# Performance work log

Measured on AMD Instinct MI355X. Metric: run time of the kernel, lower is better.

Reference implementation:

```python
import jax, jax.numpy as jnp
import numpy as np
import math

# config constants (match init_kwargs)
N_HEAD = 16
KNN_NUM = 4
MEM_FRAC = 4.0
BOOKKEEPING_FRAC = 0.0
RESID_ONLY = False
RESID_FOUND = 0.5   # set_resid_frac(resid_frac): found/current mix
RESID_CURR = 0.5
KNN_INFLUENCE = 1.0
NEG_INF = jnp.finfo(jnp.float32).min


def setup_inputs() -> dict:
    key = jax.random.key(0)
    k1, k2, k3, k4, k5 = jax.random.split(key, 5)
    B, T, C = 1, 2048, 1024
    H, d = N_HEAD, C // N_HEAD
    M = 8192  # per-head memory-store entries
    return {
        "x": jax.random.normal(k1, (B, T, C), jnp.float32),
        "c_attn_w": jax.random.normal(k2, (3 * C, C), jnp.float32) * 0.02,
        "c_proj_w": jax.random.normal(k3, (C, C), jnp.float32) * 0.02,
        "key_store": jax.random.normal(k4, (H, M, d), jnp.float32),
        "value_store": jax.random.normal(k5, (H, M, d), jnp.float32),
    }


def _knn_get(att, k, q, v, key_store, value_store):
    # att: (B,H,T,T), k/q/v: (B,H,T,d), stores: (H,M,d). B must be 1 (original
    # scatter offset i*t is only consistent for b==1).
    B, H, T, d = k.shape
    scale = 1.0 / math.sqrt(d)
    att_last = att[:, :, -1, :]                     # (B,H,T) last-query column
    # bookkeeping_frac == 0.0 -> skipped; mem_frac truthy -> threshold filter
    mask = att_last >= (1.0 / (MEM_FRAC * T))       # nonzero after zeroing

    # per-head flattened token lists, shape (H, N=B*T, d)
    kh = jnp.swapaxes(k, 0, 1).reshape(H, B * T, d)
    qh = jnp.swapaxes(q, 0, 1).reshape(H, B * T, d)
    vh = jnp.swapaxes(v, 0, 1).reshape(H, B * T, d)
    mask_h = jnp.swapaxes(mask, 0, 1).reshape(H, B * T)

    # exact L2 kNN (FAISS IndexFlatL2 equivalent): d2[h,n,m] = ||kh - ks||^2
    d2 = (jnp.sum(kh * kh, -1)[:, :, None]
          - 2.0 * jnp.einsum('hnd,hmd->hnm', kh, key_store)
          + jnp.sum(key_store * key_store, -1)[:, None, :])
    _, idx = jax.lax.top_k(-d2, KNN_NUM)            # (H,N,K) nearest indices

    h_ix = jnp.arange(H)[:, None, None]
    keys_found = key_store[h_ix, idx]               # (H,N,K,d)
    vals_found = value_store[h_ix, idx]
    keys_found = jnp.moveaxis(keys_found, 2, 0)     # (K,H,N,d)
    vals_found = jnp.moveaxis(vals_found, 2, 0)
    if not RESID_ONLY:
        keys_found = jnp.concatenate([kh[None], keys_found], axis=0)  # (K+1,H,N,d)
        vals_found = jnp.concatenate([vh[None], vals_found], axis=0)

    attf = jnp.einsum('khnd,hnd->khn', keys_found, qh) * scale
    attf = jnp.where(jnp.isnan(attf), NEG_INF, attf)
    attf = jax.nn.softmax(attf * KNN_INFLUENCE, axis=0)
    vals_new = jnp.einsum('khn,khnd->hnd', attf, vals_found)
    if RESID_FOUND > 0 or RESID_CURR > 0:
        vals_new = vals_new * RESID_FOUND + vh * RESID_CURR

    v_out = jnp.where(mask_h[..., None], vals_new, vh)   # scatter-equivalent
    return jnp.swapaxes(v_out.reshape(H, B, T, d), 0, 1)  # (B,H,T,d)


def reference(x, c_attn_w, c_proj_w, key_store, value_store):
    B, T, C = x.shape
    H, d = N_HEAD, C // N_HEAD
    qkv = x @ c_attn_w.T                             # (B,T,3C)
    q, k, v = jnp.split(qkv, 3, axis=2)
    q = jnp.swapaxes(q.reshape(B, T, H, d), 1, 2)    # (B,H,T,d)
    k = jnp.swapaxes(k.reshape(B, T, H, d), 1, 2)
    v = jnp.swapaxes(v.reshape(B, T, H, d), 1, 2)

    att = jnp.einsum('bhqd,bhkd->bhqk', q, k) * (1.0 / math.sqrt(d))
    causal = jnp.tril(jnp.ones((T, T), bool))
    att = jnp.where(causal, att, NEG_INF)
    att = jax.nn.softmax(att, axis=-1)

    # knn_get is @torch.no_grad() in the original -> stop_gradient
    v_new = jax.lax.stop_gradient(
        _knn_get(att, k, q, v, key_store, value_store))

    y = jnp.einsum('bhqk,bhkd->bhqd', att, v_new)
    y = jnp.swapaxes(y, 1, 2).reshape(B, T, C)
    return y @ c_proj_w.T
```

## Files before the change

### kernel.cpp

```cpp
#include <hip/hip_runtime.h>
#include <hip/hip_bf16.h>
#include <math.h>

#define TT 2048
#define CC 1024
#define HH 16
#define DDIM 64
#define MM 8192
#define C3 3072
#define SBIAS 256.0f

typedef __bf16 bf16x8 __attribute__((ext_vector_type(8)));
typedef float f32x4 __attribute__((ext_vector_type(4)));

__device__ __forceinline__ float waveReduceSum(float v) {
#pragma unroll
  for (int off = 32; off > 0; off >>= 1) v += __shfl_xor(v, off, 64);
  return v;
}
__device__ __forceinline__ unsigned umn(unsigned a, unsigned b){ return a<b?a:b; }
__device__ __forceinline__ unsigned umed3(unsigned a, unsigned b, unsigned c){
  unsigned d;
  asm("v_med3_u32 %0, %1, %2, %3" : "=v"(d) : "v"(a), "v"(b), "v"(c));
  return d;
}

__device__ __forceinline__ void gload16(const void* g, void* l) {
  __builtin_amdgcn_global_load_lds(
      (const __attribute__((address_space(1))) unsigned int*)g,
      (__attribute__((address_space(3))) unsigned int*)l, 16, 0, 0);
}

__global__ __launch_bounds__(256) void conv_split_k(const float* __restrict__ src,
    __hip_bfloat16* __restrict__ hi, __hip_bfloat16* __restrict__ lo)
{
  size_t i = (size_t)blockIdx.x*256 + threadIdx.x;
  const float4* p = (const float4*)(src + i*8);
  float4 a = p[0], b = p[1];
  float v[8] = {a.x,a.y,a.z,a.w,b.x,b.y,b.z,b.w};
  bf16x8 H, L;
#pragma unroll
  for (int e = 0; e < 8; ++e) {
    __bf16 hb = (__bf16)v[e];
    H[e] = hb;
    L[e] = (__bf16)(v[e] - (float)hb);
  }
  *reinterpret_cast<bf16x8*>(hi + i*8) = H;
  *reinterpret_cast<bf16x8*>(lo + i*8) = L;
}

__global__ __launch_bounds__(256) void conv_bf16_k(const float* __restrict__ src,
    __hip_bfloat16* __restrict__ dst)
{
  size_t i = (size_t)blockIdx.x*256 + threadIdx.x;
  const float4* p = (const float4*)(src + i*8);
  float4 a = p[0], b = p[1];
  float v[8] = {a.x,a.y,a.z,a.w,b.x,b.y,b.z,b.w};
  bf16x8 H;
#pragma unroll
  for (int e = 0; e < 8; ++e) H[e] = (__bf16)v[e];
  *reinterpret_cast<bf16x8*>(dst + i*8) = H;
}

__global__ __launch_bounds__(256) void conv_ks_k(const float* __restrict__ ks,
    __hip_bfloat16* __restrict__ ksb, float* __restrict__ ksn, float* __restrict__ ksnb)
{
  int row = blockIdx.x*4 + (threadIdx.x>>6);
  int lane = threadIdx.x & 63;
  float v = ks[(size_t)row*64 + lane];
  float sq = waveReduceSum(v*v);
  ksb[(size_t)row*64 + lane] = __float2bfloat16(v);
  if (lane == 0) { ksn[row] = sq; ksnb[row] = sq + SBIAS; }
}

__global__ __launch_bounds__(256) void conv_kb_k(const float* __restrict__ qkv,
    __hip_bfloat16* __restrict__ kb)
{
  int e = blockIdx.x*256 + threadIdx.x;
  int dg = e & 7; int t = (e>>3) & (TT-1); int h = e >> 14;
  const float* src = qkv + (size_t)t*C3 + CC + h*64 + dg*8;
  __hip_bfloat16* dst = kb + ((size_t)(h*TT + t)*64 + dg*8);
#pragma unroll
  for (int i = 0; i < 8; ++i) dst[i] = __float2bfloat16(src[i]);
}

__global__ __launch_bounds__(256) void vtrans_k(const float* __restrict__ vnew,
    __hip_bfloat16* __restrict__ vbT)
{
  __shared__ float tbuf[64][65];
  const int h = blockIdx.y, t0 = blockIdx.x*64, tid = threadIdx.x;
#pragma unroll
  for (int r = 0; r < 16; ++r) {
    int e = r*256 + tid; int row = e>>6, dv = e&63;
    tbuf[row][dv] = vnew[((size_t)h*TT + t0 + row)*64 + dv];
  }
  __syncthreads();
#pragma unroll
  for (int r = 0; r < 16; ++r) {
    int e = r*256 + tid; int dv = e>>6, tt = e&63;
    vbT[((size_t)h*64 + dv)*TT + t0 + tt] = __float2bfloat16(tbuf[tt][dv]);
  }
}

template<bool SPLIT>
__global__ __launch_bounds__(256) void gemm_mfma_k(
    const __hip_bfloat16* __restrict__ Ah, const __hip_bfloat16* __restrict__ Al,
    const __hip_bfloat16* __restrict__ Bh, const __hip_bfloat16* __restrict__ Bl,
    float* __restrict__ Cc, int M, int N, int K)
{
  __shared__ __align__(16) char lds[2][32768];
  const int tid = threadIdx.x;
  const int nbx = N >> 7;
  const int by = blockIdx.x / nbx, bx = blockIdx.x - by*nbx;
  const int m0 = by << 7, n0 = bx << 7;
  const int w = tid >> 6;
  const int l = tid & 63;
  const int wslot = w << 6;
  const int wi = w >> 1, wj = w & 1;
  const int fr = l & 15, fo = l >> 4;
  const int kw = SPLIT ? 32 : 64;
  const int nsteps = K / kw;

  f32x4 acc[4][4];
#pragma unroll
  for (int i = 0; i < 4; ++i)
#pragma unroll
    for (int j = 0; j < 4; ++j) acc[i][j] = f32x4{0.f,0.f,0.f,0.f};

  int srow[4], schg[4];
#pragma unroll
  for (int r = 0; r < 4; ++r) {
    int s = r*256 + tid;
    srow[r] = s >> 3;
    schg[r] = (s & 7) ^ (srow[r] & 7);
  }

  auto stageAB = [&](int buf, int st) {
    const int k0 = st * kw;
#pragma unroll
    for (int r = 0; r < 4; ++r) {
      const __hip_bfloat16 *pa, *pb;
      if (SPLIT) {
        pa = (schg[r] < 4 ? Ah : Al) + (size_t)(m0+srow[r])*K + k0 + (schg[r]&3)*8;
        pb = (schg[r] < 4 ? Bh : Bl) + (size_t)(n0+srow[r])*K + k0 + (schg[r]&3)*8;
      } else {
        pa = Ah + (size_t)(m0+srow[r])*K + k0 + schg[r]*8;
        pb = Bh + (size_t)(n0+srow[r])*K + k0 + schg[r]*8;
      }
      gload16(pa, lds[buf] + (r*256 + wslot)*16);
      gload16(pb, lds[buf] + 16384 + (r*256 + wslot)*16);
    }
  };

  stageAB(0, 0);
  __syncthreads();

  for (int st = 0; st < nsteps; ++st) {
    const int buf = st & 1;
    if (st + 1 < nsteps) stageAB(buf ^ 1, st + 1);
    char* ldsb = lds[buf];

    if (SPLIT) {
      bf16x8 bhf[4], blf[4];
#pragma unroll
      for (int j = 0; j < 4; ++j) {
        int row = wj*64 + j*16 + fr;
        bhf[j] = *(const bf16x8*)(ldsb + 16384 + row*128 + ((fo     ^ (row&7))*16));
        blf[j] = *(const bf16x8*)(ldsb + 16384 + row*128 + (((4+fo) ^ (row&7))*16));
      }
#pragma unroll
      for (int i = 0; i < 4; ++i) {
        int row = wi*64 + i*16 + fr;
        bf16x8 ah = *(const bf16x8*)(ldsb + row*128 + ((fo     ^ (row&7))*16));
        bf16x8 al = *(const bf16x8*)(ldsb + row*128 + (((4+fo) ^ (row&7))*16));
#pragma unroll
        for (int j = 0; j < 4; ++j) {
          acc[i][j] = __builtin_amdgcn_mfma_f32_16x16x32_bf16(al, bhf[j], acc[i][j], 0,0,0);
          acc[i][j] = __builtin_amdgcn_mfma_f32_16x16x32_bf16(ah, blf[j], acc[i][j], 0,0,0);
          acc[i][j] = __builtin_amdgcn_mfma_f32_16x16x32_bf16(ah, bhf[j], acc[i][j], 0,0,0);
        }
      }
    } else {
#pragma unroll
      for (int kk = 0; kk < 2; ++kk) {
        bf16x8 bf[4];
#pragma unroll
        for (int j = 0; j < 4; ++j) {
          int row = wj*64 + j*16 + fr;
          bf[j] = *(const bf16x8*)(ldsb + 16384 + row*128 + (((kk*4+fo) ^ (row&7))*16));
        }
#pragma unroll
        for (int i = 0; i < 4; ++i) {
          int row = wi*64 + i*16 + fr;
          bf16x8 af = *(const bf16x8*)(ldsb + row*128 + (((kk*4+fo) ^ (row&7))*16));
#pragma unroll
          for (int j = 0; j < 4; ++j)
            acc[i][j] = __builtin_amdgcn_mfma_f32_16x16x32_bf16(af, bf[j], acc[i][j], 0,0,0);
        }
      }
    }
    __syncthreads();
  }

  float* ep = (float*)((char*)lds + (size_t)w*8704);
#pragma unroll
  for (int pass = 0; pass < 2; ++pass) {
#pragma unroll
    for (int ii = 0; ii < 2; ++ii) {
      int i = pass*2 + ii;
#pragma unroll
      for (int j = 0; j < 4; ++j)
#pragma unroll
        for (int e = 0; e < 4; ++e)
          ep[(ii*16 + fo*4 + e)*68 + j*16 + fr] = acc[i][j][e];
    }
#pragma unroll
    for (int eidx = 0; eidx < 8; ++eidx) {
      int fi = eidx*64 + l;
      int row = fi >> 4, c4 = fi & 15;
      float4 v4 = *(const float4*)(ep + row*68 + c4*4);
      *(float4*)(Cc + (size_t)(m0 + wi*64 + pass*32 + row)*N + n0 + wj*64 + c4*4) = v4;
    }
  }
}

__global__ __launch_bounds__(256) void attlast_mask_k(const float* __restrict__ qkv, int* __restrict__ mask)
{
  const int h = blockIdx.x;
  __shared__ float ql[64];
  __shared__ float lg[TT];
  __shared__ float red[256];
  const int tid = threadIdx.x;
  if (tid < 64) ql[tid] = qkv[(size_t)(TT-1)*C3 + h*DDIM + tid];
  __syncthreads();
  float lmax = -INFINITY;
  for (int t = tid; t < TT; t += 256) {
    const float* kr = qkv + (size_t)t*C3 + CC + h*DDIM;
    float s = 0.f;
#pragma unroll
    for (int d = 0; d < 64; ++d) s += ql[d] * kr[d];
    s *= 0.125f;
    lg[t] = s;
    lmax = fmaxf(lmax, s);
  }
  red[tid] = lmax; __syncthreads();
  for (int off = 128; off > 0; off >>= 1) { if (tid < off) red[tid] = fmaxf(red[tid], red[tid+off]); __syncthreads(); }
  float mx = red[0];
  __syncthreads();
  float ls = 0.f;
  for (int t = tid; t < TT; t += 256) { float e = expf(lg[t]-mx); lg[t] = e; ls += e; }
  red[tid] = ls; __syncthreads();
  for (int off = 128; off > 0; off >>= 1) { if (tid < off) red[tid] += red[tid+off]; __syncthreads(); }
  float Z = red[0];
  for (int t = tid; t < TT; t += 256) mask[h*TT + t] = (lg[t]/Z >= 1.220703125e-4f) ? 1 : 0;
}

__global__ __launch_bounds__(256) void knn_chunkmin_k(
    const __hip_bfloat16* __restrict__ kb, const __hip_bfloat16* __restrict__ ksb,
    const float* __restrict__ ksnb, unsigned int* __restrict__ cand)
{
  __shared__ __align__(16) char lds[32768];
  const int tid = threadIdx.x;
  const int bid = blockIdx.x;
  const int orig = (bid & 7)*128 + (bid >> 3);
  const int h  = orig >> 6;
  const int n0 = (orig & 63) * 32;
  const int w  = tid >> 6;
  const int wh = w >> 1;
  const int wr = w & 1;
  const int l  = tid & 63;
  const int cr = l & 15, hi = l >> 4;

  bf16x8 af0, af1;
  {
    const __hip_bfloat16* kbh = kb + (size_t)h*TT*64 + (size_t)(n0 + wr*16 + cr)*64;
    af0 = *reinterpret_cast<const bf16x8*>(kbh + hi*8);
    af1 = *reinterpret_cast<const bf16x8*>(kbh + 32 + hi*8);
  }
  const __hip_bfloat16* ksbh = ksb + (size_t)h*MM*64;
  const float* ksnh = ksnb + (size_t)h*MM;

  char* myhalf = lds + wh*16384;
  int gsrc[4];
#pragma unroll
  for (int r = 0; r < 4; ++r) {
    int s = r*128 + wr*64 + l;
    gsrc[r] = (s & ~7) | ((s & 7) ^ ((s >> 3) & 7));
  }
  const int rb0 = cr*128 + ((hi ^ (l&7))*16);
  const int rb1 = cr*128 + (((4+hi) ^ (l&7))*16);

  unsigned cnd[4][4];
#pragma unroll
  for (int i = 0; i < 4; ++i)
#pragma unroll
    for (int c = 0; c < 4; ++c) cnd[i][c] = 0xFFFFFFFFu;

  auto stage = [&](int buf, int tt) {
    const __hip_bfloat16* src = ksbh + ((size_t)(wh*64 + tt))*4096;
    char* dst = myhalf + buf*8192 + (wr << 10);
#pragma unroll
    for (int r = 0; r < 4; ++r)
      gload16(src + gsrc[r]*8, dst + (r << 11));
  };

  stage(0, 0);
  __syncthreads();

  for (int tt = 0; tt < 64; ++tt) {
    const int buf = tt & 1;
    if (tt + 1 < 64) stage(buf ^ 1, tt + 1);
    char* ldsb = myhalf + buf*8192;
    const int ttg = wh*64 + tt;
    const unsigned crtt = ((unsigned)cr << 7) | (unsigned)ttg;

    float kn0 = ksnh[ttg*64 +  0 + cr];
    float kn1 = ksnh[ttg*64 + 16 + cr];
    float kn2 = ksnh[ttg*64 + 32 + cr];
    float kn3 = ksnh[ttg*64 + 48 + cr];

    f32x4 acc[4];
#pragma unroll
    for (int b = 0; b < 4; ++b) {
      bf16x8 bf0 = *reinterpret_cast<const bf16x8*>(ldsb + b*2048 + rb0);
      bf16x8 bf1 = *reinterpret_cast<const bf16x8*>(ldsb + b*2048 + rb1);
      f32x4 z = {0.f, 0.f, 0.f, 0.f};
      z = __builtin_amdgcn_mfma_f32_16x16x32_bf16(af0, bf0, z, 0, 0, 0);
      z = __builtin_amdgcn_mfma_f32_16x16x32_bf16(af1, bf1, z, 0, 0, 0);
      acc[b] = z;
    }
#pragma unroll
    for (int i = 0; i < 4; ++i) {
      float s0 = fmaf(acc[0][i], -2.f, kn0);
      float s1 = fmaf(acc[1][i], -2.f, kn1);
      float s2 = fmaf(acc[2][i], -2.f, kn2);
      float s3 = fmaf(acc[3][i], -2.f, kn3);
      float m4 = fminf(fminf(s0, s1), fminf(s2, s3));
      unsigned x = (__float_as_uint(m4) & 0xFFFFF800u) | crtt;
      unsigned t0 = umn(cnd[i][0], x);
      unsigned t1 = umed3(x, cnd[i][0], cnd[i][1]);
      unsigned t2 = umed3(x, cnd[i][1], cnd[i][2]);
      unsigned t3 = umed3(x, cnd[i][2], cnd[i][3]);
      cnd[i][0] = t0; cnd[i][1] = t1; cnd[i][2] = t2; cnd[i][3] = t3;
    }
    __syncthreads();
  }

  uint4* sh = (uint4*)lds;
  if (wh == 1) {
#pragma unroll
    for (int i = 0; i < 4; ++i)
      sh[wr*256 + (hi*4+i)*16 + cr] = make_uint4(cnd[i][0], cnd[i][1], cnd[i][2], cnd[i][3]);
  }
  __syncthreads();
  if (wh == 0) {
#pragma unroll
    for (int i = 0; i < 4; ++i) {
      uint4 b = sh[wr*256 + (hi*4+i)*16 + cr];
      int n = n0 + wr*16 + hi*4 + i;
      reinterpret_cast<uint4*>(cand)[(size_t)(h*TT + n)*16 + cr] =
          make_uint4(umn(cnd[i][0], b.w), umn(cnd[i][1], b.z),
                     umn(cnd[i][2], b.y), umn(cnd[i][3], b.x));
    }
  }
}

__global__ __launch_bounds__(256) void knn_fused_k(
    const unsigned int* __restrict__ cand, const float* __restrict__ qkv,
    const float* __restrict__ kstore, const float* __restrict__ vstore,
    const float* __restrict__ ksn, const int* __restrict__ mask,
    float* __restrict__ vnew)
{
  const int row = blockIdx.x*4 + (threadIdx.x>>6);
  const int l = threadIdx.x & 63;
  const int ll = l & 31;
  const int h = row >> 11, t = row & (TT-1);
  const float* base = qkv + (size_t)t*C3 + h*64;
  float vh = base[2*CC + l];
  float* outp = vnew + (size_t)row*64;
  if (!mask[row]) { outp[l] = vh; return; }

  unsigned v = cand[(size_t)row*64 + l];
#pragma unroll
  for (int k = 2; k <= 64; k <<= 1)
#pragma unroll
    for (int j = k>>1; j > 0; j >>= 1) {
      unsigned o = __shfl_xor(v, j, 64);
      bool takeMin = ((l & j) == 0) == ((l & k) == 0);
      v = (takeMin == (o < v)) ? o : v;
    }

  const int c = l >> 1;
  const int b = c & 3;
  unsigned vc = __shfl(v, c >> 2, 64);
  const int m = ((int)(vc & 127u))*64 + b*16 + (int)((vc >> 7) & 15u);
  const int p = l & 1;
  unsigned kh, km;
  {
    const float* kq = base + CC + p*32;
    const float* ksr = kstore + ((size_t)h*MM + m)*64 + p*32;
    float dp = 0.f;
#pragma unroll
    for (int i = 0; i < 8; ++i) {
      float4 a = *(const float4*)(kq + i*4);
      float4 bb = *(const float4*)(ksr + i*4);
      dp = fmaf(a.x,bb.x, fmaf(a.y,bb.y, fmaf(a.z,bb.z, fmaf(a.w,bb.w, dp))));
    }
    dp += __shfl_xor(dp, 1, 64);
    float s = ksn[(size_t)h*MM + m] - 2.f*dp;
    unsigned u = __float_as_uint(s);
    unsigned skey = u ^ (unsigned)(((int)u >> 31) | 0x80000000);
    kh = __shfl(skey, 2*ll, 64);
    km = __shfl((unsigned)m, 2*ll, 64);
#pragma unroll
    for (int k = 2; k <= 32; k <<= 1)
#pragma unroll
      for (int j = k>>1; j > 0; j >>= 1) {
        unsigned oh = __shfl_xor(kh, j, 64);
        unsigned ol = __shfl_xor(km, j, 64);
        bool takeMin = ((ll & j) == 0) == ((ll & k) == 0);
        bool oLess = (oh < kh) || (oh == kh && ol < km);
        if (takeMin == oLess) { kh = oh; km = ol; }
      }
  }

  const int m0 = (int)__shfl(km, 0, 64);
  const int m1 = (int)__shfl(km, 1, 64);
  const int m2 = (int)__shfl(km, 2, 64);
  const int m3 = (int)__shfl(km, 3, 64);
  const int g = l >> 3, gl = l & 7;
  float dq = 0.f;
  if (g < 5) {
    int msel = (g == 0) ? m0 : (g == 1) ? m1 : (g == 2) ? m2 : m3;
    const float* qrow = base + gl*8;
    const float* kr = (g < 4) ? (kstore + ((size_t)h*MM + msel)*64 + gl*8)
                              : (base + CC + gl*8);
    float4 a0 = *(const float4*)(qrow);
    float4 a1 = *(const float4*)(qrow + 4);
    float4 b0 = *(const float4*)(kr);
    float4 b1 = *(const float4*)(kr + 4);
    dq = a0.x*b0.x + a0.y*b0.y + a0.z*b0.z + a0.w*b0.w
       + a1.x*b1.x + a1.y*b1.y + a1.z*b1.z + a1.w*b1.w;
  }
  dq += __shfl_xor(dq, 1, 64);
  dq += __shfl_xor(dq, 2, 64);
  dq += __shfl_xor(dq, 4, 64);
  float d0 = __shfl(dq,  0, 64)*0.125f;
  float d1 = __shfl(dq,  8, 64)*0.125f;
  float d2 = __shfl(dq, 16, 64)*0.125f;
  float d3 = __shfl(dq, 24, 64)*0.125f;
  float d4 = __shfl(dq, 32, 64)*0.125f;
  float mx = fmaxf(fmaxf(fmaxf(d0,d1),fmaxf(d2,d3)),d4);
  float w0 = __expf(d0-mx), w1 = __expf(d1-mx), w2 = __expf(d2-mx),
        w3 = __expf(d3-mx), w4 = __expf(d4-mx);
  float Z = w0+w1+w2+w3+w4;
  float vv = w4*vh
           + w0*vstore[((size_t)h*MM+m0)*64 + l]
           + w1*vstore[((size_t)h*MM+m1)*64 + l]
           + w2*vstore[((size_t)h*MM+m2)*64 + l]
           + w3*vstore[((size_t)h*MM+m3)*64 + l];
  outp[l] = 0.5f*(vv/Z) + 0.5f*vh;
}

__global__ __launch_bounds__(256) void attn_mfma_k(
    const float* __restrict__ qkv, const __hip_bfloat16* __restrict__ kb,
    const __hip_bfloat16* __restrict__ vbT, __hip_bfloat16* __restrict__ yb)
{
  __shared__ __align__(16) char lds[40960];
  const int h = blockIdx.y, bx = blockIdx.x, tid = threadIdx.x;
  const int w = tid>>6, l = tid&63, fr = l&15, fo = l>>4;
  const int wslot = w << 6;
  const __hip_bfloat16* kbh = kb + (size_t)h*TT*64;
  const __hip_bfloat16* vbh = vbT + (size_t)h*64*TT;
  char* Pt = lds + 32768 + w*2048;

  int srow[2], schg[2];
#pragma unroll
  for (int r = 0; r < 2; ++r) {
    int s = r*256 + tid;
    srow[r] = s >> 3;
    schg[r] = (s & 7) ^ (srow[r] & 7);
  }

  auto stageKV = [&](int buf, int kt) {
#pragma unroll
    for (int r = 0; r < 2; ++r) {
      gload16(kbh + (size_t)(kt*64 + srow[r])*64 + schg[r]*8,
              lds + buf*16384 + (r*256 + wslot)*16);
      gload16(vbh + (size_t)srow[r]*TT + kt*64 + schg[r]*8,
              lds + buf*16384 + 8192 + (r*256 + wslot)*16);
    }
  };

  const int qblk = 31 - bx;
  const int q0 = qblk * 64;
  bf16x8 qa[2];
  {
    const float* qrow = qkv + (size_t)(q0 + w*16 + fr)*C3 + h*64;
#pragma unroll
    for (int kk = 0; kk < 2; ++kk) {
      float4 u0 = *(const float4*)(qrow + kk*32 + fo*8);
      float4 u1 = *(const float4*)(qrow + kk*32 + fo*8 + 4);
      bf16x8 t;
      t[0]=(__bf16)u0.x; t[1]=(__bf16)u0.y; t[2]=(__bf16)u0.z; t[3]=(__bf16)u0.w;
      t[4]=(__bf16)u1.x; t[5]=(__bf16)u1.y; t[6]=(__bf16)u1.z; t[7]=(__bf16)u1.w;
      qa[kk] = t;
    }
  }
  float mrow[4], lsum[4];
  f32x4 oacc[4];
#pragma unroll
  for (int e = 0; e < 4; ++e) { mrow[e] = -INFINITY; lsum[e] = 0.f; }
#pragma unroll
  for (int jv = 0; jv < 4; ++jv) oacc[jv] = f32x4{0.f,0.f,0.f,0.f};

  const int ntiles = qblk + 1;
  stageKV(0, 0);
  __syncthreads();

  for (int kt = 0; kt < ntiles; ++kt) {
    const int buf = kt & 1;
    if (kt + 1 < ntiles) stageKV(buf ^ 1, kt + 1);
    char* Kt = lds + buf*16384;
    char* Vt = Kt + 8192;

    f32x4 sv[4];
#pragma unroll
    for (int j = 0; j < 4; ++j) {
      int row = j*16 + fr;
      bf16x8 k0f = *(const bf16x8*)(Kt + row*128 + ((fo     ^ (row&7))*16));
      bf16x8 k1f = *(const bf16x8*)(Kt + row*128 + (((4+fo) ^ (row&7))*16));
      f32x4 z = {0.f,0.f,0.f,0.f};
      z = __builtin_amdgcn_mfma_f32_16x16x32_bf16(qa[0], k0f, z, 0,0,0);
      z = __builtin_amdgcn_mfma_f32_16x16x32_bf16(qa[1], k1f, z, 0,0,0);
      sv[j] = z;
    }
    if (kt == qblk) {
#pragma unroll
      for (int j = 0; j < 4; ++j)
#pragma unroll
        for (int e = 0; e < 4; ++e)
          sv[j][e] = (j*16 + fr <= w*16 + fo*4 + e) ? sv[j][e]*0.125f : -INFINITY;
    } else {
#pragma unroll
      for (int j = 0; j < 4; ++j)
#pragma unroll
        for (int e = 0; e < 4; ++e) sv[j][e] *= 0.125f;
    }
    float rmax[4];
#pragma unroll
    for (int e = 0; e < 4; ++e)
      rmax[e] = fmaxf(fmaxf(sv[0][e], sv[1][e]), fmaxf(sv[2][e], sv[3][e]));
#pragma unroll
    for (int off = 1; off < 16; off <<= 1)
#pragma unroll
      for (int e = 0; e < 4; ++e) rmax[e] = fmaxf(rmax[e], __shfl_xor(rmax[e], off, 64));
    float scl[4];
#pragma unroll
    for (int e = 0; e < 4; ++e) {
      float mn = fmaxf(mrow[e], rmax[e]);
      scl[e] = __expf(mrow[e] - mn);
      mrow[e] = mn;
    }
    float rsum[4] = {0.f,0.f,0.f,0.f};
#pragma unroll
    for (int j = 0; j < 4; ++j) {
      int chunkbase = j*2 + (fr>>3);
      int kvoff = (fr&7)*2;
#pragma unroll
      for (int e = 0; e < 4; ++e) {
        float p = __expf(sv[j][e] - mrow[e]);
        rsum[e] += p;
        int qloc = fo*4 + e;
        *(__bf16*)(Pt + qloc*128 + ((chunkbase ^ (qloc&7))*16) + kvoff) = (__bf16)p;
      }
    }
#pragma unroll
    for (int off = 1; off < 16; off <<= 1)
#pragma unroll
      for (int e = 0; e < 4; ++e) rsum[e] += __shfl_xor(rsum[e], off, 64);
#pragma unroll
    for (int e = 0; e < 4; ++e) lsum[e] = lsum[e]*scl[e] + rsum[e];
#pragma unroll
    for (int jv = 0; jv < 4; ++jv)
#pragma unroll
      for (int e = 0; e < 4; ++e) oacc[jv][e] *= scl[e];

    bf16x8 pa0 = *(const bf16x8*)(Pt + fr*128 + ((fo     ^ (fr&7))*16));
    bf16x8 pa1 = *(const bf16x8*)(Pt + fr*128 + (((4+fo) ^ (fr&7))*16));
#pragma unroll
    for (int jv = 0; jv < 4; ++jv) {
      int row = jv*16 + fr;
      bf16x8 v0f = *(const bf16x8*)(Vt + row*128 + ((fo     ^ (row&7))*16));
      bf16x8 v1f = *(const bf16x8*)(Vt + row*128 + (((4+fo) ^ (row&7))*16));
      oacc[jv] = __builtin_amdgcn_mfma_f32_16x16x32_bf16(pa0, v0f, oacc[jv], 0,0,0);
      oacc[jv] = __builtin_amdgcn_mfma_f32_16x16x32_bf16(pa1, v1f, oacc[jv], 0,0,0);
    }
    __syncthreads();
  }
#pragma unroll
  for (int jv = 0; jv < 4; ++jv)
#pragma unroll
    for (int e = 0; e < 4; ++e) {
      int t = q0 + w*16 + fo*4 + e;
      yb[(size_t)t*CC + h*64 + jv*16 + fr] = __float2bfloat16(oacc[jv][e] / lsum[e]);
    }
}

extern "C" void kernel_launch(void* const* d_in, const int* in_sizes, int n_in,
                              void* d_out, int out_size, void* d_ws, size_t ws_size,
                              hipStream_t stream) {
  const float* x   = (const float*)d_in[0];
  const float* wat = (const float*)d_in[1];
  const float* wpr = (const float*)d_in[2];
  const float* kst = (const float*)d_in[3];
  const float* vst = (const float*)d_in[4];
  float* out = (float*)d_out;

  float* ws    = (float*)d_ws;
  float* qkv   = ws;
  float* ksn   = qkv + (size_t)6291456;
  float* ksnb  = ksn + 131072;
  int*   idxb  = (int*)(ksnb + 131072);
  int*   maskb = idxb + 131072;
  __hip_bfloat16* kb = (__hip_bfloat16*)(maskb + 32768);
  float* candRegion = (float*)kb + 1048576;
  unsigned int* candb = (unsigned int*)candRegion;
  float* vnew = candRegion;
  __hip_bfloat16* vbT = (__hip_bfloat16*)(candRegion + 2097152);
  float* split = candRegion + 2097152 + 1048576;
  __hip_bfloat16* xhi = (__hip_bfloat16*)split;
  __hip_bfloat16* xlo = xhi + 2097152;
  __hip_bfloat16* whi = xlo + 2097152;
  __hip_bfloat16* wlo = whi + 3145728;
  __hip_bfloat16* ksb  = (__hip_bfloat16*)split;
  __hip_bfloat16* wprb = ksb + 8388608;
  __hip_bfloat16* yb   = (__hip_bfloat16*)split;

  conv_split_k<<<dim3(1024), 256, 0, stream>>>(x, xhi, xlo);
  conv_split_k<<<dim3(1536), 256, 0, stream>>>(wat, whi, wlo);
  gemm_mfma_k<true><<<dim3(16*24), 256, 0, stream>>>(xhi, xlo, whi, wlo, qkv, TT, C3, CC);
  conv_kb_k<<<dim3(1024), 256, 0, stream>>>(qkv, kb);
  conv_ks_k<<<dim3(HH*MM/4), 256, 0, stream>>>(kst, ksb, ksn, ksnb);
  conv_bf16_k<<<dim3(512), 256, 0, stream>>>(wpr, wprb);
  attlast_mask_k<<<dim3(HH), 256, 0, stream>>>(qkv, maskb);
  knn_chunkmin_k<<<dim3(1024), 256, 0, stream>>>(kb, ksb, ksnb, candb);
  knn_fused_k<<<dim3(HH*TT/4), 256, 0, stream>>>(candb, qkv, kst, vst, ksn, maskb, vnew);
  vtrans_k<<<dim3(32, HH), 256, 0, stream>>>(vnew, vbT);
  attn_mfma_k<<<dim3(32, HH), 256, 0, stream>>>(qkv, kb, vbT, yb);
  gemm_mfma_k<false><<<dim3(16*8), 256, 0, stream>>>(yb, nullptr, wprb, nullptr, out, TT, CC, CC);
}
```

Measured before the change: 314.3 us.

## Merge conversion kernels, transpose key-norm layout, pair causal attention blocks

Folds the two split conversions into one launch, and folds the attention-mask, key-store conversion, K conversion and proj-weight conversion into a single multi-role kernel. This cuts launch count and lets independent small jobs run concurrently. Key-store norms are written in a transposed layout so the kNN kernel fetches four norms with one float4 load instead of four scalar loads. The causal attention kernel now processes a short and a long query block per workgroup (bx and 31-bx), which balances work across 256 blocks, at the cost of fewer blocks and serialised halves.

```diff
diff --git a/kernel.cpp b/kernel.cpp
--- a/kernel.cpp
+++ b/kernel.cpp
@@ -31,10 +31,9 @@
       (__attribute__((address_space(3))) unsigned int*)l, 16, 0, 0);
 }
 
-__global__ __launch_bounds__(256) void conv_split_k(const float* __restrict__ src,
-    __hip_bfloat16* __restrict__ hi, __hip_bfloat16* __restrict__ lo)
-{
-  size_t i = (size_t)blockIdx.x*256 + threadIdx.x;
+__device__ __forceinline__ void conv_split_body(const float* __restrict__ src,
+    __hip_bfloat16* __restrict__ hi, __hip_bfloat16* __restrict__ lo, size_t i)
+{
   const float4* p = (const float4*)(src + i*8);
   float4 a = p[0], b = p[1];
   float v[8] = {a.x,a.y,a.z,a.w,b.x,b.y,b.z,b.w};
@@ -49,10 +48,9 @@
   *reinterpret_cast<bf16x8*>(lo + i*8) = L;
 }
 
-__global__ __launch_bounds__(256) void conv_bf16_k(const float* __restrict__ src,
-    __hip_bfloat16* __restrict__ dst)
-{
-  size_t i = (size_t)blockIdx.x*256 + threadIdx.x;
+__device__ __forceinline__ void conv_bf16_body(const float* __restrict__ src,
+    __hip_bfloat16* __restrict__ dst, size_t i)
+{
   const float4* p = (const float4*)(src + i*8);
   float4 a = p[0], b = p[1];
   float v[8] = {a.x,a.y,a.z,a.w,b.x,b.y,b.z,b.w};
@@ -62,26 +60,73 @@
   *reinterpret_cast<bf16x8*>(dst + i*8) = H;
 }
 
-__global__ __launch_bounds__(256) void conv_ks_k(const float* __restrict__ ks,
-    __hip_bfloat16* __restrict__ ksb, float* __restrict__ ksn, float* __restrict__ ksnb)
-{
-  int row = blockIdx.x*4 + (threadIdx.x>>6);
-  int lane = threadIdx.x & 63;
-  float v = ks[(size_t)row*64 + lane];
-  float sq = waveReduceSum(v*v);
-  ksb[(size_t)row*64 + lane] = __float2bfloat16(v);
-  if (lane == 0) { ksn[row] = sq; ksnb[row] = sq + SBIAS; }
-}
-
-__global__ __launch_bounds__(256) void conv_kb_k(const float* __restrict__ qkv,
-    __hip_bfloat16* __restrict__ kb)
-{
-  int e = blockIdx.x*256 + threadIdx.x;
-  int dg = e & 7; int t = (e>>3) & (TT-1); int h = e >> 14;
-  const float* src = qkv + (size_t)t*C3 + CC + h*64 + dg*8;
-  __hip_bfloat16* dst = kb + ((size_t)(h*TT + t)*64 + dg*8);
-#pragma unroll
-  for (int i = 0; i < 8; ++i) dst[i] = __float2bfloat16(src[i]);
+__global__ __launch_bounds__(256) void mega1_k(
+    const float* __restrict__ x, __hip_bfloat16* __restrict__ xhi, __hip_bfloat16* __restrict__ xlo,
+    const float* __restrict__ wat, __hip_bfloat16* __restrict__ whi, __hip_bfloat16* __restrict__ wlo)
+{
+  int bid = blockIdx.x;
+  if (bid < 1024) conv_split_body(x, xhi, xlo, (size_t)bid*256 + threadIdx.x);
+  else            conv_split_body(wat, whi, wlo, (size_t)(bid-1024)*256 + threadIdx.x);
+}
+
+__global__ __launch_bounds__(256) void mega2_k(
+    const float* __restrict__ qkv, int* __restrict__ mask,
+    const float* __restrict__ kst, __hip_bfloat16* __restrict__ ksb,
+    float* __restrict__ ksn, float* __restrict__ ksnbT,
+    __hip_bfloat16* __restrict__ kb,
+    const float* __restrict__ wpr, __hip_bfloat16* __restrict__ wprb)
+{
+  __shared__ float sm[64 + TT + 256];
+  const int bid = blockIdx.x;
+  const int tid = threadIdx.x;
+  if (bid < 16) {
+    const int h = bid;
+    float* ql = sm;
+    float* lg = sm + 64;
+    float* red = sm + 64 + TT;
+    if (tid < 64) ql[tid] = qkv[(size_t)(TT-1)*C3 + h*DDIM + tid];
+    __syncthreads();
+    float lmax = -INFINITY;
+    for (int t = tid; t < TT; t += 256) {
+      const float* kr = qkv + (size_t)t*C3 + CC + h*DDIM;
+      float s = 0.f;
+#pragma unroll
+      for (int d = 0; d < 64; ++d) s += ql[d] * kr[d];
+      s *= 0.125f;
+      lg[t] = s;
+      lmax = fmaxf(lmax, s);
+    }
+    red[tid] = lmax; __syncthreads();
+    for (int off = 128; off > 0; off >>= 1) { if (tid < off) red[tid] = fmaxf(red[tid], red[tid+off]); __syncthreads(); }
+    float mx = red[0];
+    __syncthreads();
+    float ls = 0.f;
+    for (int t = tid; t < TT; t += 256) { float e = expf(lg[t]-mx); lg[t] = e; ls += e; }
+    red[tid] = ls; __syncthreads();
+    for (int off = 128; off > 0; off >>= 1) { if (tid < off) red[tid] += red[tid+off]; __syncthreads(); }
+    float Z = red[0];
+    for (int t = tid; t < TT; t += 256) mask[h*TT + t] = (lg[t]/Z >= 1.220703125e-4f) ? 1 : 0;
+  } else if (bid < 16 + 32768) {
+    int row = (bid - 16)*4 + (tid>>6);
+    int lane = tid & 63;
+    float v = kst[(size_t)row*64 + lane];
+    float sq = waveReduceSum(v*v);
+    ksb[(size_t)row*64 + lane] = __float2bfloat16(v);
+    if (lane == 0) {
+      ksn[row] = sq;
+      int m = row & (MM-1), h = row >> 13;
+      ksnbT[(((size_t)h*16 + (m & 15))*128 + (m >> 6))*4 + ((m >> 4) & 3)] = sq + SBIAS;
+    }
+  } else if (bid < 16 + 32768 + 1024) {
+    int e = (bid - 16 - 32768)*256 + tid;
+    int dg = e & 7; int t = (e>>3) & (TT-1); int h = e >> 14;
+    const float* src = qkv + (size_t)t*C3 + CC + h*64 + dg*8;
+    __hip_bfloat16* dst = kb + ((size_t)(h*TT + t)*64 + dg*8);
+#pragma unroll
+    for (int i = 0; i < 8; ++i) dst[i] = __float2bfloat16(src[i]);
+  } else {
+    conv_bf16_body(wpr, wprb, (size_t)(bid - 33808)*256 + tid);
+  }
 }
 
 __global__ __launch_bounds__(256) void vtrans_k(const float* __restrict__ vnew,
@@ -132,7 +177,7 @@
   for (int r = 0; r < 4; ++r) {
     int s = r*256 + tid;
     srow[r] = s >> 3;
-    schg[r] = (s & 7) ^ (srow[r] & 7);
+    schg[r] = (s & 7) ^ ((s >> 3) & 7);
   }
 
   auto stageAB = [&](int buf, int st) {
@@ -224,40 +269,9 @@
   }
 }
 
-__global__ __launch_bounds__(256) void attlast_mask_k(const float* __restrict__ qkv, int* __restrict__ mask)
-{
-  const int h = blockIdx.x;
-  __shared__ float ql[64];
-  __shared__ float lg[TT];
-  __shared__ float red[256];
-  const int tid = threadIdx.x;
-  if (tid < 64) ql[tid] = qkv[(size_t)(TT-1)*C3 + h*DDIM + tid];
-  __syncthreads();
-  float lmax = -INFINITY;
-  for (int t = tid; t < TT; t += 256) {
-    const float* kr = qkv + (size_t)t*C3 + CC + h*DDIM;
-    float s = 0.f;
-#pragma unroll
-    for (int d = 0; d < 64; ++d) s += ql[d] * kr[d];
-    s *= 0.125f;
-    lg[t] = s;
-    lmax = fmaxf(lmax, s);
-  }
-  red[tid] = lmax; __syncthreads();
-  for (int off = 128; off > 0; off >>= 1) { if (tid < off) red[tid] = fmaxf(red[tid], red[tid+off]); __syncthreads(); }
-  float mx = red[0];
-  __syncthreads();
-  float ls = 0.f;
-  for (int t = tid; t < TT; t += 256) { float e = expf(lg[t]-mx); lg[t] = e; ls += e; }
-  red[tid] = ls; __syncthreads();
-  for (int off = 128; off > 0; off >>= 1) { if (tid < off) red[tid] += red[tid+off]; __syncthreads(); }
-  float Z = red[0];
-  for (int t = tid; t < TT; t += 256) mask[h*TT + t] = (lg[t]/Z >= 1.220703125e-4f) ? 1 : 0;
-}
-
 __global__ __launch_bounds__(256) void knn_chunkmin_k(
     const __hip_bfloat16* __restrict__ kb, const __hip_bfloat16* __restrict__ ksb,
-    const float* __restrict__ ksnb, unsigned int* __restrict__ cand)
+    const float* __restrict__ ksnbT, unsigned int* __restrict__ cand)
 {
   __shared__ __align__(16) char lds[32768];
   const int tid = threadIdx.x;
@@ -278,7 +292,7 @@
     af1 = *reinterpret_cast<const bf16x8*>(kbh + 32 + hi*8);
   }
   const __hip_bfloat16* ksbh = ksb + (size_t)h*MM*64;
-  const float* ksnh = ksnb + (size_t)h*MM;
+  const float4* knp = (const float4*)ksnbT + ((size_t)h*16 + cr)*128;
 
   char* myhalf = lds + wh*16384;
   int gsrc[4];
@@ -314,10 +328,7 @@
     const int ttg = wh*64 + tt;
     const unsigned crtt = ((unsigned)cr << 7) | (unsigned)ttg;
 
-    float kn0 = ksnh[ttg*64 +  0 + cr];
-    float kn1 = ksnh[ttg*64 + 16 + cr];
-    float kn2 = ksnh[ttg*64 + 32 + cr];
-    float kn3 = ksnh[ttg*64 + 48 + cr];
+    float4 kn = knp[ttg];
 
     f32x4 acc[4];
 #pragma unroll
@@ -331,10 +342,10 @@
     }
 #pragma unroll
     for (int i = 0; i < 4; ++i) {
-      float s0 = fmaf(acc[0][i], -2.f, kn0);
-      float s1 = fmaf(acc[1][i], -2.f, kn1);
-      float s2 = fmaf(acc[2][i], -2.f, kn2);
-      float s3 = fmaf(acc[3][i], -2.f, kn3);
+      float s0 = fmaf(acc[0][i], -2.f, kn.x);
+      float s1 = fmaf(acc[1][i], -2.f, kn.y);
+      float s2 = fmaf(acc[2][i], -2.f, kn.z);
+      float s3 = fmaf(acc[3][i], -2.f, kn.w);
       float m4 = fminf(fminf(s0, s1), fminf(s2, s3));
       unsigned x = (__float_as_uint(m4) & 0xFFFFF800u) | crtt;
       unsigned t0 = umn(cnd[i][0], x);
@@ -479,7 +490,7 @@
   for (int r = 0; r < 2; ++r) {
     int s = r*256 + tid;
     srow[r] = s >> 3;
-    schg[r] = (s & 7) ^ (srow[r] & 7);
+    schg[r] = (s & 7) ^ ((s >> 3) & 7);
   }
 
   auto stageKV = [&](int buf, int kt) {
@@ -492,119 +503,121 @@
     }
   };
 
-  const int qblk = 31 - bx;
-  const int q0 = qblk * 64;
-  bf16x8 qa[2];
-  {
-    const float* qrow = qkv + (size_t)(q0 + w*16 + fr)*C3 + h*64;
-#pragma unroll
-    for (int kk = 0; kk < 2; ++kk) {
-      float4 u0 = *(const float4*)(qrow + kk*32 + fo*8);
-      float4 u1 = *(const float4*)(qrow + kk*32 + fo*8 + 4);
-      bf16x8 t;
-      t[0]=(__bf16)u0.x; t[1]=(__bf16)u0.y; t[2]=(__bf16)u0.z; t[3]=(__bf16)u0.w;
-      t[4]=(__bf16)u1.x; t[5]=(__bf16)u1.y; t[6]=(__bf16)u1.z; t[7]=(__bf16)u1.w;
-      qa[kk] = t;
-    }
-  }
-  float mrow[4], lsum[4];
-  f32x4 oacc[4];
-#pragma unroll
-  for (int e = 0; e < 4; ++e) { mrow[e] = -INFINITY; lsum[e] = 0.f; }
-#pragma unroll
-  for (int jv = 0; jv < 4; ++jv) oacc[jv] = f32x4{0.f,0.f,0.f,0.f};
-
-  const int ntiles = qblk + 1;
-  stageKV(0, 0);
-  __syncthreads();
-
-  for (int kt = 0; kt < ntiles; ++kt) {
-    const int buf = kt & 1;
-    if (kt + 1 < ntiles) stageKV(buf ^ 1, kt + 1);
-    char* Kt = lds + buf*16384;
-    char* Vt = Kt + 8192;
-
-    f32x4 sv[4];
-#pragma unroll
-    for (int j = 0; j < 4; ++j) {
-      int row = j*16 + fr;
-      bf16x8 k0f = *(const bf16x8*)(Kt + row*128 + ((fo     ^ (row&7))*16));
-      bf16x8 k1f = *(const bf16x8*)(Kt + row*128 + (((4+fo) ^ (row&7))*16));
-      f32x4 z = {0.f,0.f,0.f,0.f};
-      z = __builtin_amdgcn_mfma_f32_16x16x32_bf16(qa[0], k0f, z, 0,0,0);
-      z = __builtin_amdgcn_mfma_f32_16x16x32_bf16(qa[1], k1f, z, 0,0,0);
-      sv[j] = z;
-    }
-    if (kt == qblk) {
-#pragma unroll
-      for (int j = 0; j < 4; ++j)
-#pragma unroll
-        for (int e = 0; e < 4; ++e)
-          sv[j][e] = (j*16 + fr <= w*16 + fo*4 + e) ? sv[j][e]*0.125f : -INFINITY;
-    } else {
-#pragma unroll
-      for (int j = 0; j < 4; ++j)
-#pragma unroll
-        for (int e = 0; e < 4; ++e) sv[j][e] *= 0.125f;
-    }
-    float rmax[4];
-#pragma unroll
-    for (int e = 0; e < 4; ++e)
-      rmax[e] = fmaxf(fmaxf(sv[0][e], sv[1][e]), fmaxf(sv[2][e], sv[3][e]));
-#pragma unroll
-    for (int off = 1; off < 16; off <<= 1)
-#pragma unroll
-      for (int e = 0; e < 4; ++e) rmax[e] = fmaxf(rmax[e], __shfl_xor(rmax[e], off, 64));
-    float scl[4];
-#pragma unroll
-    for (int e = 0; e < 4; ++e) {
-      float mn = fmaxf(mrow[e], rmax[e]);
-      scl[e] = __expf(mrow[e] - mn);
-      mrow[e] = mn;
-    }
-    float rsum[4] = {0.f,0.f,0.f,0.f};
-#pragma unroll
-    for (int j = 0; j < 4; ++j) {
-      int chunkbase = j*2 + (fr>>3);
-      int kvoff = (fr&7)*2;
+  for (int half = 0; half < 2; ++half) {
+    const int qblk = half ? (31 - bx) : bx;
+    const int q0 = qblk * 64;
+    bf16x8 qa[2];
+    {
+      const float* qrow = qkv + (size_t)(q0 + w*16 + fr)*C3 + h*64;
+#pragma unroll
+      for (int kk = 0; kk < 2; ++kk) {
+        float4 u0 = *(const float4*)(qrow + kk*32 + fo*8);
+        float4 u1 = *(const float4*)(qrow + kk*32 + fo*8 + 4);
+        bf16x8 t;
+        t[0]=(__bf16)u0.x; t[1]=(__bf16)u0.y; t[2]=(__bf16)u0.z; t[3]=(__bf16)u0.w;
+        t[4]=(__bf16)u1.x; t[5]=(__bf16)u1.y; t[6]=(__bf16)u1.z; t[7]=(__bf16)u1.w;
+        qa[kk] = t;
+      }
+    }
+    float mrow[4], lsum[4];
+    f32x4 oacc[4];
+#pragma unroll
+    for (int e = 0; e < 4; ++e) { mrow[e] = -INFINITY; lsum[e] = 0.f; }
+#pragma unroll
+    for (int jv = 0; jv < 4; ++jv) oacc[jv] = f32x4{0.f,0.f,0.f,0.f};
+
+    const int ntiles = qblk + 1;
+    stageKV(0, 0);
+    __syncthreads();
+
+    for (int kt = 0; kt < ntiles; ++kt) {
+      const int buf = kt & 1;
+      if (kt + 1 < ntiles) stageKV(buf ^ 1, kt + 1);
+      char* Kt = lds + buf*16384;
+      char* Vt = Kt + 8192;
+
+      f32x4 sv[4];
+#pragma unroll
+      for (int j = 0; j < 4; ++j) {
+        int row = j*16 + fr;
+        bf16x8 k0f = *(const bf16x8*)(Kt + row*128 + ((fo     ^ (row&7))*16));
+        bf16x8 k1f = *(const bf16x8*)(Kt + row*128 + (((4+fo) ^ (row&7))*16));
+        f32x4 z = {0.f,0.f,0.f,0.f};
+        z = __builtin_amdgcn_mfma_f32_16x16x32_bf16(qa[0], k0f, z, 0,0,0);
+        z = __builtin_amdgcn_mfma_f32_16x16x32_bf16(qa[1], k1f, z, 0,0,0);
+        sv[j] = z;
+      }
+      if (kt == qblk) {
+#pragma unroll
+        for (int j = 0; j < 4; ++j)
+#pragma unroll
+          for (int e = 0; e < 4; ++e)
+            sv[j][e] = (j*16 + fr <= w*16 + fo*4 + e) ? sv[j][e]*0.125f : -INFINITY;
+      } else {
+#pragma unroll
+        for (int j = 0; j < 4; ++j)
+#pragma unroll
+          for (int e = 0; e < 4; ++e) sv[j][e] *= 0.125f;
+      }
+      float rmax[4];
+#pragma unroll
+      for (int e = 0; e < 4; ++e)
+        rmax[e] = fmaxf(fmaxf(sv[0][e], sv[1][e]), fmaxf(sv[2][e], sv[3][e]));
+#pragma unroll
+      for (int off = 1; off < 16; off <<= 1)
+#pragma unroll
+        for (int e = 0; e < 4; ++e) rmax[e] = fmaxf(rmax[e], __shfl_xor(rmax[e], off, 64));
+      float scl[4];
 #pragma unroll
       for (int e = 0; e < 4; ++e) {
-        float p = __expf(sv[j][e] - mrow[e]);
-        rsum[e] += p;
-        int qloc = fo*4 + e;
-        *(__bf16*)(Pt + qloc*128 + ((chunkbase ^ (qloc&7))*16) + kvoff) = (__bf16)p;
-      }
-    }
-#pragma unroll
-    for (int off = 1; off < 16; off <<= 1)
-#pragma unroll
-      for (int e = 0; e < 4; ++e) rsum[e] += __shfl_xor(rsum[e], off, 64);
-#pragma unroll
-    for (int e = 0; e < 4; ++e) lsum[e] = lsum[e]*scl[e] + rsum[e];
+        float mn = fmaxf(mrow[e], rmax[e]);
+        scl[e] = __expf(mrow[e] - mn);
+        mrow[e] = mn;
+      }
+      float rsum[4] = {0.f,0.f,0.f,0.f};
+#pragma unroll
+      for (int j = 0; j < 4; ++j) {
+        int chunkbase = j*2 + (fr>>3);
+        int kvoff = (fr&7)*2;
+#pragma unroll
+        for (int e = 0; e < 4; ++e) {
+          float p = __expf(sv[j][e] - mrow[e]);
+          rsum[e] += p;
+          int qloc = fo*4 + e;
+          *(__bf16*)(Pt + qloc*128 + ((chunkbase ^ (qloc&7))*16) + kvoff) = (__bf16)p;
+        }
+      }
+#pragma unroll
+      for (int off = 1; off < 16; off <<= 1)
+#pragma unroll
+        for (int e = 0; e < 4; ++e) rsum[e] += __shfl_xor(rsum[e], off, 64);
+#pragma unroll
+      for (int e = 0; e < 4; ++e) lsum[e] = lsum[e]*scl[e] + rsum[e];
+#pragma unroll
+      for (int jv = 0; jv < 4; ++jv)
+#pragma unroll
+        for (int e = 0; e < 4; ++e) oacc[jv][e] *= scl[e];
+
+      bf16x8 pa0 = *(const bf16x8*)(Pt + fr*128 + ((fo     ^ (fr&7))*16));
+      bf16x8 pa1 = *(const bf16x8*)(Pt + fr*128 + (((4+fo) ^ (fr&7))*16));
+#pragma unroll
+      for (int jv = 0; jv < 4; ++jv) {
+        int row = jv*16 + fr;
+        bf16x8 v0f = *(const bf16x8*)(Vt + row*128 + ((fo     ^ (row&7))*16));
+        bf16x8 v1f = *(const bf16x8*)(Vt + row*128 + (((4+fo) ^ (row&7))*16));
+        oacc[jv] = __builtin_amdgcn_mfma_f32_16x16x32_bf16(pa0, v0f, oacc[jv], 0,0,0);
+        oacc[jv] = __builtin_amdgcn_mfma_f32_16x16x32_bf16(pa1, v1f, oacc[jv], 0,0,0);
+      }
+      __syncthreads();
+    }
 #pragma unroll
     for (int jv = 0; jv < 4; ++jv)
 #pragma unroll
-      for (int e = 0; e < 4; ++e) oacc[jv][e] *= scl[e];
-
-    bf16x8 pa0 = *(const bf16x8*)(Pt + fr*128 + ((fo     ^ (fr&7))*16));
-    bf16x8 pa1 = *(const bf16x8*)(Pt + fr*128 + (((4+fo) ^ (fr&7))*16));
-#pragma unroll
-    for (int jv = 0; jv < 4; ++jv) {
-      int row = jv*16 + fr;
-      bf16x8 v0f = *(const bf16x8*)(Vt + row*128 + ((fo     ^ (row&7))*16));
-      bf16x8 v1f = *(const bf16x8*)(Vt + row*128 + (((4+fo) ^ (row&7))*16));
-      oacc[jv] = __builtin_amdgcn_mfma_f32_16x16x32_bf16(pa0, v0f, oacc[jv], 0,0,0);
-      oacc[jv] = __builtin_amdgcn_mfma_f32_16x16x32_bf16(pa1, v1f, oacc[jv], 0,0,0);
-    }
-    __syncthreads();
-  }
-#pragma unroll
-  for (int jv = 0; jv < 4; ++jv)
-#pragma unroll
-    for (int e = 0; e < 4; ++e) {
-      int t = q0 + w*16 + fo*4 + e;
-      yb[(size_t)t*CC + h*64 + jv*16 + fr] = __float2bfloat16(oacc[jv][e] / lsum[e]);
-    }
+      for (int e = 0; e < 4; ++e) {
+        int t = q0 + w*16 + fo*4 + e;
+        yb[(size_t)t*CC + h*64 + jv*16 + fr] = __float2bfloat16(oacc[jv][e] / lsum[e]);
+      }
+  }
 }
 
 extern "C" void kernel_launch(void* const* d_in, const int* in_sizes, int n_in,
@@ -620,8 +633,8 @@
   float* ws    = (float*)d_ws;
   float* qkv   = ws;
   float* ksn   = qkv + (size_t)6291456;
-  float* ksnb  = ksn + 131072;
-  int*   idxb  = (int*)(ksnb + 131072);
+  float* ksnbT = ksn + 131072;
+  int*   idxb  = (int*)(ksnbT + 131072);
   int*   maskb = idxb + 131072;
   __hip_bfloat16* kb = (__hip_bfloat16*)(maskb + 32768);
   float* candRegion = (float*)kb + 1048576;
@@ -637,16 +650,12 @@
   __hip_bfloat16* wprb = ksb + 8388608;
   __hip_bfloat16* yb   = (__hip_bfloat16*)split;
 
-  conv_split_k<<<dim3(1024), 256, 0, stream>>>(x, xhi, xlo);
-  conv_split_k<<<dim3(1536), 256, 0, stream>>>(wat, whi, wlo);
+  mega1_k<<<dim3(2560), 256, 0, stream>>>(x, xhi, xlo, wat, whi, wlo);
   gemm_mfma_k<true><<<dim3(16*24), 256, 0, stream>>>(xhi, xlo, whi, wlo, qkv, TT, C3, CC);
-  conv_kb_k<<<dim3(1024), 256, 0, stream>>>(qkv, kb);
-  conv_ks_k<<<dim3(HH*MM/4), 256, 0, stream>>>(kst, ksb, ksn, ksnb);
-  conv_bf16_k<<<dim3(512), 256, 0, stream>>>(wpr, wprb);
-  attlast_mask_k<<<dim3(HH), 256, 0, stream>>>(qkv, maskb);
-  knn_chunkmin_k<<<dim3(1024), 256, 0, stream>>>(kb, ksb, ksnb, candb);
+  mega2_k<<<dim3(34320), 256, 0, stream>>>(qkv, maskb, kst, ksb, ksn, ksnbT, kb, wpr, wprb);
+  knn_chunkmin_k<<<dim3(1024), 256, 0, stream>>>(kb, ksb, ksnbT, candb);
   knn_fused_k<<<dim3(HH*TT/4), 256, 0, stream>>>(candb, qkv, kst, vst, ksn, maskb, vnew);
   vtrans_k<<<dim3(32, HH), 256, 0, stream>>>(vnew, vbT);
-  attn_mfma_k<<<dim3(32, HH), 256, 0, stream>>>(qkv, kb, vbT, yb);
+  attn_mfma_k<<<dim3(16, HH), 256, 0, stream>>>(qkv, kb, vbT, yb);
   gemm_mfma_k<false><<<dim3(16*8), 256, 0, stream>>>(yb, nullptr, wprb, nullptr, out, TT, CC, CC);
 }
```

After: 292.0 us. 1.08x faster.
